# Kernel optimization log

Measured on AMD Instinct MI355X. Metric: run time of the kernel, lower is better.

## Reference

```python
import jax, jax.numpy as jnp
import numpy as np

EPS = 1e-5

def conv2d(x, w, stride=1, pad=0, groups=1):
    return jax.lax.conv_general_dilated(
        x, w, (stride, stride), [(pad, pad), (pad, pad)],
        feature_group_count=groups,
        dimension_numbers=('NCHW', 'OIHW', 'NCHW'))

def prelu(x, a):
    return jnp.where(x > 0, x, a[None, :, None, None] * x)

def batchnorm(x, g, b):
    # training-mode BN: batch statistics over N,H,W (biased variance, as torch)
    m = jnp.mean(x, axis=(0, 2, 3), keepdims=True)
    v = jnp.var(x, axis=(0, 2, 3), keepdims=True)
    xhat = (x - m) * jax.lax.rsqrt(v + EPS)
    return xhat * g[None, :, None, None] + b[None, :, None, None]

def setup_inputs() -> dict:
    key = jax.random.key(0)
    ks = jax.random.split(key, 8)
    C_in, C_out, stride = 128, 256, 2
    x = jax.random.normal(ks[0], (32, C_in, 56, 56), dtype=jnp.float32)
    w1 = jax.random.normal(ks[1], (C_out, C_in, 1, 1), dtype=jnp.float32) * 0.05
    w_dw = jax.random.normal(ks[2], (C_out, 1, 3, 3), dtype=jnp.float32) * 0.1
    w3 = jax.random.normal(ks[3], (C_out, C_out, 1, 1), dtype=jnp.float32) * 0.05
    w_adj = jax.random.normal(ks[4], (C_out, C_in, 1, 1), dtype=jnp.float32) * 0.05
    a_init = jnp.full((C_out,), 0.25, dtype=jnp.float32)  # PReLU init
    ones = jnp.ones((C_out,), dtype=jnp.float32)
    zeros = jnp.zeros((C_out,), dtype=jnp.float32)
    return {
        'x': x,
        'w1': w1, 'a1': a_init, 'g1': ones, 'b1': zeros,
        'w_dw': w_dw, 'a2': a_init, 'g2': ones, 'b2': zeros,
        'w3': w3, 'a3': a_init, 'g3': ones, 'b3': zeros,
        'w_adj': w_adj,
    }

def reference(x, w1, a1, g1, b1, w_dw, a2, g2, b2, w3, a3, g3, b3, w_adj):
    stride, C_out = 2, w_dw.shape[0]
    residual = conv2d(x, w_adj, stride=stride)  # full-precision shortcut
    xs = jnp.sign(x)
    # binary 1x1 conv (sign(x) already signed; sign is idempotent)
    out = conv2d(jnp.sign(xs), jnp.sign(w1))
    out = batchnorm(prelu(out, a1), g1, b1)
    # binary depthwise 3x3, stride, pad 1
    out = conv2d(jnp.sign(out), jnp.sign(w_dw), stride=stride, pad=1, groups=C_out)
    out = batchnorm(prelu(out, a2), g2, b2)
    # binary 1x1 conv
    out = conv2d(jnp.sign(out), jnp.sign(w3))
    out = batchnorm(prelu(out, a3), g3, b3)
    return out + residual
```

## Files before the change

### kernel.cpp

```cpp
#include <hip/hip_runtime.h>
#include <stdint.h>

#define NB   32
#define CIN  128
#define COUT 256
#define HH   56
#define WW   56
#define S1   (HH*WW)
#define HO   28
#define WO   28
#define S2   (HO*WO)
#define NS1  (NB*S1)
#define NS2  (NB*S2)
#define TOT2 (NS2*COUT)
#define EPSV 1e-5f

constexpr size_t OFF_XBITS = 0;
constexpr size_t OFF_WB1   = OFF_XBITS + (size_t)NS1*8*4;
constexpr size_t OFF_WB3   = OFF_WB1 + 256*8*4;
constexpr size_t OFF_WDW   = OFF_WB3 + 256*16*4;
constexpr size_t OFF_ACC   = OFF_WDW + 4096;
constexpr size_t OFF_WBADJ = OFF_ACC + 3*256*4*sizeof(int);
constexpr size_t OFF_XG    = OFF_WBADJ + (size_t)COUT*CIN*2;
constexpr size_t OFF_OUT1  = OFF_XG + (size_t)NS2*CIN*2;
constexpr size_t OFF_OUT2  = OFF_OUT1 + (size_t)NS1*COUT;
constexpr size_t OFF_XB2   = OFF_OUT2 + (size_t)TOT2;
constexpr size_t OFF_OUT3  = OFF_XB2 + (size_t)NS2*16*4;

typedef __attribute__((ext_vector_type(8))) short bf16x8;
typedef __attribute__((ext_vector_type(4))) float f32x4;

__device__ __forceinline__ uint32_t f2bf(float v) {
  uint32_t u = __float_as_uint(v);
  return (u + 0x7fffu + ((u >> 16) & 1u)) >> 16;
}

__device__ __forceinline__ void bn_finalize(const int* __restrict__ acc4,
                                            float a, float g, float b, float inv_ns,
                                            float& sc, float& sh) {
  float ps = (float)acc4[0];
  float ng = (float)acc4[1];
  float pq = (float)acc4[2];
  float nq = (float)acc4[3];
  float mean = (ps + a*ng) * inv_ns;
  float ex2  = (pq + a*a*nq) * inv_ns;
  float var  = ex2 - mean*mean;
  float rs   = rsqrtf(var + EPSV);
  sc = rs * g;
  sh = b - mean * sc;
}

__global__ __launch_bounds__(256) void packx_kernel(
    const float* __restrict__ x, uint32_t* __restrict__ xbits,
    uint32_t* __restrict__ xg,
    const float* __restrict__ w1, const float* __restrict__ w3,
    const float* __restrict__ wdw, const float* __restrict__ wadj,
    uint32_t* __restrict__ wb1, uint32_t* __restrict__ wb3,
    int8_t* __restrict__ wdws, uint32_t* __restrict__ wbadj,
    int* __restrict__ accbase) {
  int wdx = blockIdx.y;
  if (wdx == 0 && blockIdx.x < 256 && threadIdx.x < 64) {
    int co = blockIdx.x;
    int l  = threadIdx.x;
    if (l < 12) {
      int set = l >> 2, k = l & 3;
      accbase[set*1024 + co*4 + k] = 0;
    }
    for (int h = 0; h < 2; ++h) {
      float v = w1[(size_t)co*CIN + h*64 + l];
      unsigned long long bp = __ballot(v > 0.f);
      unsigned long long bn = __ballot(v < 0.f);
      if (l == 0) {
        wb1[co*8 + 2*h    ] = (uint32_t)bp;
        wb1[co*8 + 2*h + 1] = (uint32_t)(bp >> 32);
        wb1[co*8 + 4 + 2*h    ] = (uint32_t)bn;
        wb1[co*8 + 4 + 2*h + 1] = (uint32_t)(bn >> 32);
      }
    }
    for (int h = 0; h < 4; ++h) {
      float v = w3[(size_t)co*COUT + h*64 + l];
      unsigned long long bp = __ballot(v > 0.f);
      unsigned long long bn = __ballot(v < 0.f);
      if (l == 0) {
        wb3[co*16 + 2*h    ] = (uint32_t)bp;
        wb3[co*16 + 2*h + 1] = (uint32_t)(bp >> 32);
        wb3[co*16 + 8 + 2*h    ] = (uint32_t)bn;
        wb3[co*16 + 8 + 2*h + 1] = (uint32_t)(bn >> 32);
      }
    }
    if (l < 9) {
      float v = wdw[co*9 + l];
      wdws[co*9 + l] = (int8_t)((v > 0.f) - (v < 0.f));
    }
    {
      float v0 = wadj[(size_t)co*CIN + 2*l];
      float v1 = wadj[(size_t)co*CIN + 2*l + 1];
      wbadj[co*64 + l] = f2bf(v0) | (f2bf(v1) << 16);
    }
  }

  int m = blockIdx.x*256 + threadIdx.x;
  int n = m / S1, hw = m % S1;
  size_t base = ((size_t)n*CIN + wdx*32)*S1 + hw;
  uint32_t p = 0, q = 0;
  uint32_t bv[16];
  #pragma unroll
  for (int j = 0; j < 32; ++j) {
    float v = x[base + (size_t)j*S1];
    p |= (uint32_t)(v > 0.f) << j;
    q |= (uint32_t)(v < 0.f) << j;
    uint32_t b = f2bf(v);
    if (j & 1) bv[j >> 1] |= b << 16; else bv[j >> 1] = b;
  }
  xbits[(size_t)m*8 + wdx    ] = p;
  xbits[(size_t)m*8 + 4 + wdx] = q;
  int h = hw / WW, w = hw % WW;
  if (((h | w) & 1) == 0) {
    int m2 = n*S2 + (h >> 1)*WO + (w >> 1);
    uint4* dst = (uint4*)(xg + (size_t)m2*64 + wdx*16);
    dst[0] = make_uint4(bv[0],  bv[1],  bv[2],  bv[3]);
    dst[1] = make_uint4(bv[4],  bv[5],  bv[6],  bv[7]);
    dst[2] = make_uint4(bv[8],  bv[9],  bv[10], bv[11]);
    dst[3] = make_uint4(bv[12], bv[13], bv[14], bv[15]);
  }
}

__global__ __launch_bounds__(256) void conv1_kernel(
    const uint32_t* __restrict__ xb, const uint32_t* __restrict__ wb,
    int8_t* __restrict__ out1, int* __restrict__ accum1) {
  int tid = threadIdx.x;
  int qm = blockIdx.x*256 + tid;
  int m0 = qm*4;
  int n  = m0 / S1;
  int hw0 = m0 - n*S1;
  int co0 = blockIdx.y * 8;

  const uint4* xw = (const uint4*)(xb + (size_t)m0*8);
  uint4 xp0 = xw[0], xq0 = xw[1];
  uint4 xp1 = xw[2], xq1 = xw[3];
  uint4 xp2 = xw[4], xq2 = xw[5];
  uint4 xp3 = xw[6], xq3 = xw[7];

  uint32_t nz = (xp0.x|xq0.x)&(xp0.y|xq0.y)&(xp0.z|xq0.z)&(xp0.w|xq0.w)
              & (xp1.x|xq1.x)&(xp1.y|xq1.y)&(xp1.z|xq1.z)&(xp1.w|xq1.w)
              & (xp2.x|xq2.x)&(xp2.y|xq2.y)&(xp2.z|xq2.z)&(xp2.w|xq2.w)
              & (xp3.x|xq3.x)&(xp3.y|xq3.y)&(xp3.z|xq3.z)&(xp3.w|xq3.w);

  uint32_t res[8];
  if (nz == 0xffffffffu) {
    #pragma unroll
    for (int j = 0; j < 8; ++j) {
      const uint32_t* w8 = wb + (size_t)(co0 + j)*8;
      uint32_t w0 = w8[0], w1 = w8[1], w2 = w8[2], w3 = w8[3];
      int a0 = 128 - 2*(__popc(xp0.x^w0)+__popc(xp0.y^w1)+__popc(xp0.z^w2)+__popc(xp0.w^w3));
      int a1 = 128 - 2*(__popc(xp1.x^w0)+__popc(xp1.y^w1)+__popc(xp1.z^w2)+__popc(xp1.w^w3));
      int a2 = 128 - 2*(__popc(xp2.x^w0)+__popc(xp2.y^w1)+__popc(xp2.z^w2)+__popc(xp2.w^w3));
      int a3 = 128 - 2*(__popc(xp3.x^w0)+__popc(xp3.y^w1)+__popc(xp3.z^w2)+__popc(xp3.w^w3));
      if (a0 > 127) a0 = 127;
      if (a1 > 127) a1 = 127;
      if (a2 > 127) a2 = 127;
      if (a3 > 127) a3 = 127;
      res[j] = (uint32_t)(uint8_t)a0 | ((uint32_t)(uint8_t)a1 << 8)
             | ((uint32_t)(uint8_t)a2 << 16) | ((uint32_t)(uint8_t)a3 << 24);
    }
  } else {
    #pragma unroll
    for (int j = 0; j < 8; ++j) {
      const uint32_t* w8 = wb + (size_t)(co0 + j)*8;
      uint32_t w0 = w8[0], w1 = w8[1], w2 = w8[2], w3 = w8[3];
      uint32_t v0 = w8[4], v1 = w8[5], v2 = w8[6], v3 = w8[7];
      int a0 = __popc(xp0.x&w0)+__popc(xp0.y&w1)+__popc(xp0.z&w2)+__popc(xp0.w&w3)
             + __popc(xq0.x&v0)+__popc(xq0.y&v1)+__popc(xq0.z&v2)+__popc(xq0.w&v3)
             - __popc(xp0.x&v0)-__popc(xp0.y&v1)-__popc(xp0.z&v2)-__popc(xp0.w&v3)
             - __popc(xq0.x&w0)-__popc(xq0.y&w1)-__popc(xq0.z&w2)-__popc(xq0.w&w3);
      int a1 = __popc(xp1.x&w0)+__popc(xp1.y&w1)+__popc(xp1.z&w2)+__popc(xp1.w&w3)
             + __popc(xq1.x&v0)+__popc(xq1.y&v1)+__popc(xq1.z&v2)+__popc(xq1.w&v3)
             - __popc(xp1.x&v0)-__popc(xp1.y&v1)-__popc(xp1.z&v2)-__popc(xp1.w&v3)
             - __popc(xq1.x&w0)-__popc(xq1.y&w1)-__popc(xq1.z&w2)-__popc(xq1.w&w3);
      int a2 = __popc(xp2.x&w0)+__popc(xp2.y&w1)+__popc(xp2.z&w2)+__popc(xp2.w&w3)
             + __popc(xq2.x&v0)+__popc(xq2.y&v1)+__popc(xq2.z&v2)+__popc(xq2.w&v3)
             - __popc(xp2.x&v0)-__popc(xp2.y&v1)-__popc(xp2.z&v2)-__popc(xp2.w&v3)
             - __popc(xq2.x&w0)-__popc(xq2.y&w1)-__popc(xq2.z&w2)-__popc(xq2.w&w3);
      int a3 = __popc(xp3.x&w0)+__popc(xp3.y&w1)+__popc(xp3.z&w2)+__popc(xp3.w&w3)
             + __popc(xq3.x&v0)+__popc(xq3.y&v1)+__popc(xq3.z&v2)+__popc(xq3.w&v3)
             - __popc(xp3.x&v0)-__popc(xp3.y&v1)-__popc(xp3.z&v2)-__popc(xp3.w&v3)
             - __popc(xq3.x&w0)-__popc(xq3.y&w1)-__popc(xq3.z&w2)-__popc(xq3.w&w3);
      if (a0 > 127) a0 = 127;
      if (a1 > 127) a1 = 127;
      if (a2 > 127) a2 = 127;
      if (a3 > 127) a3 = 127;
      res[j] = (uint32_t)(uint8_t)a0 | ((uint32_t)(uint8_t)a1 << 8)
             | ((uint32_t)(uint8_t)a2 << 16) | ((uint32_t)(uint8_t)a3 << 24);
    }
  }

  __shared__ int sl[256][33];
  #pragma unroll
  for (int j = 0; j < 8; ++j) {
    int b0 = (int)(int8_t)(res[j]);
    int b1 = (int)(int8_t)(res[j] >> 8);
    int b2 = (int)(int8_t)(res[j] >> 16);
    int b3 = (int)(int8_t)(res[j] >> 24);
    int ps = 0, ns = 0, pq = 0, nq = 0;
    if (b0 > 0) { ps += b0; pq += b0*b0; } else { ns += b0; nq += b0*b0; }
    if (b1 > 0) { ps += b1; pq += b1*b1; } else { ns += b1; nq += b1*b1; }
    if (b2 > 0) { ps += b2; pq += b2*b2; } else { ns += b2; nq += b2*b2; }
    if (b3 > 0) { ps += b3; pq += b3*b3; } else { ns += b3; nq += b3*b3; }
    sl[tid][j*4+0] = ps; sl[tid][j*4+1] = ns;
    sl[tid][j*4+2] = pq; sl[tid][j*4+3] = nq;
  }
  __syncthreads();

  #pragma unroll
  for (int j = 0; j < 8; ++j)
    *(uint32_t*)(out1 + (size_t)(n*COUT + co0 + j)*S1 + hw0) = res[j];

  int s = tid & 31, g = tid >> 5;
  int part = 0;
  #pragma unroll
  for (int i = 0; i < 32; ++i) part += sl[g*32 + i][s];
  part += __shfl_xor(part, 32);
  __shared__ int sW[4][32];
  if ((tid & 63) < 32) sW[tid >> 6][s] = part;
  __syncthreads();
  if (tid < 32) {
    int tot = sW[0][tid] + sW[1][tid] + sW[2][tid] + sW[3][tid];
    atomicAdd(&accum1[co0*4 + tid], tot);
  }
}

#define DW_SLABS 8
#define DW_RB    68
__global__ __launch_bounds__(256) void dw_kernel(
    const int8_t* __restrict__ out1, const int8_t* __restrict__ wdws,
    const int* __restrict__ acc1, const float* __restrict__ a1,
    const float* __restrict__ g1, const float* __restrict__ b1,
    int8_t* __restrict__ out2, int* __restrict__ accum2) {
  __shared__ int8_t sl[DW_SLABS][57][DW_RB];
  __shared__ int sTp[DW_SLABS], sTn[DW_SLABS], sAcc[DW_SLABS][4];
  int tid = threadIdx.x;
  int nc0 = blockIdx.x * DW_SLABS;
  int co0 = nc0 & (COUT-1);

  int* slw = (int*)&sl[0][0][0];
  #pragma unroll
  for (int i = tid; i < DW_SLABS*57*DW_RB/4; i += 256) slw[i] = 0;
  if (tid < DW_SLABS) { sTp[tid] = 128; sTn[tid] = -129; }
  if (tid < DW_SLABS*4) sAcc[tid >> 2][tid & 3] = 0;
  __syncthreads();

  {
    int slab = tid >> 5;
    int co = co0 + slab;
    float av = a1[co], sc, sh;
    bn_finalize(acc1 + co*4, av, g1[co], b1[co], 1.f/NS1, sc, sh);
    int tp = 128, tn = -129;
    int v0 = -128 + (tid & 31)*8;
    #pragma unroll
    for (int k = 0; k < 8; ++k) {
      int v = v0 + k;
      float f = (float)v;
      float pr = f > 0.f ? f : av*f;
      float tv = pr*sc + sh;
      if (tv > 0.f && v < tp) tp = v;
      if (tv < 0.f && v > tn) tn = v;
    }
    atomicMin(&sTp[slab], tp);
    atomicMax(&sTn[slab], tn);
  }
  __syncthreads();

  for (int i = tid; i < DW_SLABS*784; i += 256) {
    int slab = i / 784;
    int d    = i - slab*784;
    int ih   = d / 14;
    int iwd  = d - ih*14;
    int Tp = sTp[slab], Tn = sTn[slab];
    uint32_t v4 = ((const uint32_t*)(out1 + (size_t)(nc0 + slab)*S1))[d];
    uint32_t s4 = 0;
    #pragma unroll
    for (int k = 0; k < 4; ++k) {
      int v = (int)(int8_t)(v4 >> (8*k));
      int s = (v >= Tp) - (v <= Tn);
      s4 |= (uint32_t)(s & 0xff) << (8*k);
    }
    *(uint32_t*)&sl[slab][ih + 1][4 + 4*iwd] = s4;
  }
  __syncthreads();

  int psum = 0, nsum = 0, psq = 0, nsq = 0;
  int slabD = tid / HO;
  if (tid < DW_SLABS*HO) {
    int ho   = tid - slabD*HO;
    int nc = nc0 + slabD;
    int co = co0 + slabD;
    int wv[9];
    #pragma unroll
    for (int k = 0; k < 9; ++k) wv[k] = wdws[co*9 + k];
    const uint32_t* r0 = (const uint32_t*)&sl[slabD][2*ho    ][4];
    const uint32_t* r1 = (const uint32_t*)&sl[slabD][2*ho + 1][4];
    const uint32_t* r2 = (const uint32_t*)&sl[slabD][2*ho + 2][4];
    uint32_t* o32 = (uint32_t*)(out2 + (size_t)nc*S2 + ho*WO);
    int c0 = 0, c1 = 0, c2 = 0;
    uint32_t obuf = 0;
    #pragma unroll
    for (int q = 0; q < 14; ++q) {
      uint32_t d0 = r0[q], d1 = r1[q], d2 = r2[q];
      int s00=(int)(int8_t)d0, s01=(int)(int8_t)(d0>>8), s02=(int)(int8_t)(d0>>16), s03=(int)(int8_t)(d0>>24);
      int s10=(int)(int8_t)d1, s11=(int)(int8_t)(d1>>8), s12=(int)(int8_t)(d1>>16), s13=(int)(int8_t)(d1>>24);
      int s20=(int)(int8_t)d2, s21=(int)(int8_t)(d2>>8), s22=(int)(int8_t)(d2>>16), s23=(int)(int8_t)(d2>>24);
      int a0 = c0*wv[0] + s00*wv[1] + s01*wv[2]
             + c1*wv[3] + s10*wv[4] + s11*wv[5]
             + c2*wv[6] + s20*wv[7] + s21*wv[8];
      int a1v = s01*wv[0] + s02*wv[1] + s03*wv[2]
              + s11*wv[3] + s12*wv[4] + s13*wv[5]
              + s21*wv[6] + s22*wv[7] + s23*wv[8];
      c0 = s03; c1 = s13; c2 = s23;
      if (a0 > 0) { psum += a0; psq += a0*a0; } else { nsum += a0; nsq += a0*a0; }
      if (a1v > 0) { psum += a1v; psq += a1v*a1v; } else { nsum += a1v; nsq += a1v*a1v; }
      if ((q & 1) == 0) {
        obuf = (uint32_t)(a0 & 0xff) | ((uint32_t)(a1v & 0xff) << 8);
      } else {
        obuf |= ((uint32_t)(a0 & 0xff) << 16) | ((uint32_t)(a1v & 0xff) << 24);
        o32[q >> 1] = obuf;
      }
    }
    atomicAdd(&sAcc[slabD][0], psum);
    atomicAdd(&sAcc[slabD][1], nsum);
    atomicAdd(&sAcc[slabD][2], psq);
    atomicAdd(&sAcc[slabD][3], nsq);
  }
  __syncthreads();

  if (tid < DW_SLABS*4) {
    int slab = tid >> 2, k = tid & 3;
    atomicAdd(&accum2[(co0 + slab)*4 + k], sAcc[slab][k]);
  }
}

__global__ __launch_bounds__(256) void pack2_kernel(
    const int8_t* __restrict__ out2, const int* __restrict__ acc2,
    const float* __restrict__ a2, const float* __restrict__ g2,
    const float* __restrict__ b2, uint32_t* __restrict__ xb2) {
  __shared__ int sTp[32], sTn[32];
  int wdx = blockIdx.y;
  if (threadIdx.x < 32) {
    int c = wdx*32 + threadIdx.x;
    float av = a2[c], sc, sh;
    bn_finalize(acc2 + c*4, av, g2[c], b2[c], 1.f/NS2, sc, sh);
    int tp = 10, tn = -10;
    for (int v = -9; v <= 9; ++v) {
      float f = (float)v;
      float pr = f > 0.f ? f : av*f;
      float tv = pr*sc + sh;
      if (tv > 0.f && v < tp) tp = v;
      if (tv < 0.f && v > tn) tn = v;
    }
    sTp[threadIdx.x] = tp; sTn[threadIdx.x] = tn;
  }
  __syncthreads();
  int m = blockIdx.x*256 + threadIdx.x;
  int n = m / S2, hw = m % S2;
  uint32_t p = 0, q = 0;
  #pragma unroll
  for (int j = 0; j < 32; ++j) {
    int c = wdx*32 + j;
    int v = out2[(size_t)(n*COUT + c)*S2 + hw];
    p |= (uint32_t)(v >= sTp[j]) << j;
    q |= (uint32_t)(v <= sTn[j]) << j;
  }
  xb2[(size_t)m*16 + wdx    ] = p;
  xb2[(size_t)m*16 + 8 + wdx] = q;
}

__global__ __launch_bounds__(256) void conv3_kernel(
    const uint32_t* __restrict__ xb2, const uint32_t* __restrict__ wb3,
    int16_t* __restrict__ out3, int* __restrict__ accum3) {
  int tid = threadIdx.x;
  int qm = blockIdx.x*256 + tid;
  int m0 = qm*2;
  int n  = m0 / S2;
  int hw0 = m0 - n*S2;
  int co0 = blockIdx.y * 8;

  const uint4* xw = (const uint4*)(xb2 + (size_t)m0*16);
  uint4 P0a = xw[0], P0b = xw[1], Q0a = xw[2], Q0b = xw[3];
  uint4 P1a = xw[4], P1b = xw[5], Q1a = xw[6], Q1b = xw[7];

  uint32_t nz = (P0a.x|Q0a.x)&(P0a.y|Q0a.y)&(P0a.z|Q0a.z)&(P0a.w|Q0a.w)
              & (P0b.x|Q0b.x)&(P0b.y|Q0b.y)&(P0b.z|Q0b.z)&(P0b.w|Q0b.w)
              & (P1a.x|Q1a.x)&(P1a.y|Q1a.y)&(P1a.z|Q1a.z)&(P1a.w|Q1a.w)
              & (P1b.x|Q1b.x)&(P1b.y|Q1b.y)&(P1b.z|Q1b.z)&(P1b.w|Q1b.w);

  uint32_t res[8];
  if (nz == 0xffffffffu) {
    #pragma unroll
    for (int j = 0; j < 8; ++j) {
      const uint32_t* w = wb3 + (size_t)(co0 + j)*16;
      int s0 = __popc(P0a.x^w[0])+__popc(P0a.y^w[1])+__popc(P0a.z^w[2])+__popc(P0a.w^w[3])
             + __popc(P0b.x^w[4])+__popc(P0b.y^w[5])+__popc(P0b.z^w[6])+__popc(P0b.w^w[7]);
      int s1 = __popc(P1a.x^w[0])+__popc(P1a.y^w[1])+__popc(P1a.z^w[2])+__popc(P1a.w^w[3])
             + __popc(P1b.x^w[4])+__popc(P1b.y^w[5])+__popc(P1b.z^w[6])+__popc(P1b.w^w[7]);
      int a0 = 256 - 2*s0, a1 = 256 - 2*s1;
      res[j] = (uint32_t)(uint16_t)(int16_t)a0 | ((uint32_t)(uint16_t)(int16_t)a1 << 16);
    }
  } else {
    #pragma unroll
    for (int j = 0; j < 8; ++j) {
      const uint32_t* w = wb3 + (size_t)(co0 + j)*16;
      int a0 = __popc(P0a.x&w[0])+__popc(P0a.y&w[1])+__popc(P0a.z&w[2])+__popc(P0a.w&w[3])
             + __popc(P0b.x&w[4])+__popc(P0b.y&w[5])+__popc(P0b.z&w[6])+__popc(P0b.w&w[7])
             + __popc(Q0a.x&w[8])+__popc(Q0a.y&w[9])+__popc(Q0a.z&w[10])+__popc(Q0a.w&w[11])
             + __popc(Q0b.x&w[12])+__popc(Q0b.y&w[13])+__popc(Q0b.z&w[14])+__popc(Q0b.w&w[15])
             - __popc(P0a.x&w[8])-__popc(P0a.y&w[9])-__popc(P0a.z&w[10])-__popc(P0a.w&w[11])
             - __popc(P0b.x&w[12])-__popc(P0b.y&w[13])-__popc(P0b.z&w[14])-__popc(P0b.w&w[15])
             - __popc(Q0a.x&w[0])-__popc(Q0a.y&w[1])-__popc(Q0a.z&w[2])-__popc(Q0a.w&w[3])
             - __popc(Q0b.x&w[4])-__popc(Q0b.y&w[5])-__popc(Q0b.z&w[6])-__popc(Q0b.w&w[7]);
      int a1 = __popc(P1a.x&w[0])+__popc(P1a.y&w[1])+__popc(P1a.z&w[2])+__popc(P1a.w&w[3])
             + __popc(P1b.x&w[4])+__popc(P1b.y&w[5])+__popc(P1b.z&w[6])+__popc(P1b.w&w[7])
             + __popc(Q1a.x&w[8])+__popc(Q1a.y&w[9])+__popc(Q1a.z&w[10])+__popc(Q1a.w&w[11])
             + __popc(Q1b.x&w[12])+__popc(Q1b.y&w[13])+__popc(Q1b.z&w[14])+__popc(Q1b.w&w[15])
             - __popc(P1a.x&w[8])-__popc(P1a.y&w[9])-__popc(P1a.z&w[10])-__popc(P1a.w&w[11])
             - __popc(P1b.x&w[12])-__popc(P1b.y&w[13])-__popc(P1b.z&w[14])-__popc(P1b.w&w[15])
             - __popc(Q1a.x&w[0])-__popc(Q1a.y&w[1])-__popc(Q1a.z&w[2])-__popc(Q1a.w&w[3])
             - __popc(Q1b.x&w[4])-__popc(Q1b.y&w[5])-__popc(Q1b.z&w[6])-__popc(Q1b.w&w[7]);
      res[j] = (uint32_t)(uint16_t)(int16_t)a0 | ((uint32_t)(uint16_t)(int16_t)a1 << 16);
    }
  }

  __shared__ int sl[256][33];
  #pragma unroll
  for (int j = 0; j < 8; ++j) {
    int b0 = (int)(int16_t)(res[j] & 0xffff);
    int b1 = (int)(int16_t)(res[j] >> 16);
    int ps = 0, ns = 0, pq = 0, nq = 0;
    if (b0 > 0) { ps += b0; pq += b0*b0; } else { ns += b0; nq += b0*b0; }
    if (b1 > 0) { ps += b1; pq += b1*b1; } else { ns += b1; nq += b1*b1; }
    sl[tid][j*4+0] = ps; sl[tid][j*4+1] = ns;
    sl[tid][j*4+2] = pq; sl[tid][j*4+3] = nq;
  }
  __syncthreads();

  #pragma unroll
  for (int j = 0; j < 8; ++j)
    *(uint32_t*)(out3 + (size_t)(n*COUT + co0 + j)*S2 + hw0) = res[j];

  int s = tid & 31, g = tid >> 5;
  int part = 0;
  #pragma unroll
  for (int i = 0; i < 32; ++i) part += sl[g*32 + i][s];
  part += __shfl_xor(part, 32);
  __shared__ int sW[4][32];
  if ((tid & 63) < 32) sW[tid >> 6][s] = part;
  __syncthreads();
  if (tid < 32) {
    int tot = sW[0][tid] + sW[1][tid] + sW[2][tid] + sW[3][tid];
    atomicAdd(&accum3[co0*4 + tid], tot);
  }
}

__global__ __launch_bounds__(256) void resfinal_kernel(
    const uint16_t* __restrict__ xg, const uint16_t* __restrict__ wb,
    const int16_t* __restrict__ out3,
    const float* __restrict__ a3, const float* __restrict__ g3,
    const float* __restrict__ b3, const int* __restrict__ acc3,
    float* __restrict__ out) {
  int lane = threadIdx.x & 63;
  int wid  = threadIdx.x >> 6;
  int m0  = blockIdx.x*64 + wid*16;
  int r16 = lane & 15, hi = lane >> 4;
  int koff = hi * 8;

  const bf16x8* arow = (const bf16x8*)(xg + (size_t)(m0 + r16)*CIN + koff);
  bf16x8 af0 = arow[0], af1 = arow[4], af2 = arow[8], af3 = arow[12];

  f32x4 dd[16];
  #pragma unroll
  for (int t = 0; t < 16; ++t) {
    const bf16x8* brow = (const bf16x8*)(wb + (size_t)(t*16 + r16)*CIN + koff);
    f32x4 a = {0.f,0.f,0.f,0.f};
    a = __builtin_amdgcn_mfma_f32_16x16x32_bf16(af0, brow[0],  a, 0,0,0);
    a = __builtin_amdgcn_mfma_f32_16x16x32_bf16(af1, brow[4],  a, 0,0,0);
    a = __builtin_amdgcn_mfma_f32_16x16x32_bf16(af2, brow[8],  a, 0,0,0);
    a = __builtin_amdgcn_mfma_f32_16x16x32_bf16(af3, brow[12], a, 0,0,0);
    dd[t] = a;
  }

  int mrow = m0 + hi*4;
  int n  = mrow / S2;
  int hw = mrow - n*S2;
  #pragma unroll
  for (int t = 0; t < 16; ++t) {
    int co = t*16 + r16;
    float av = a3[co], sc, sh;
    bn_finalize(acc3 + co*4, av, g3[co], b3[co], 1.f/NS2, sc, sh);
    size_t o = ((size_t)n*COUT + co)*S2 + hw;
    #pragma unroll
    for (int r = 0; r < 4; ++r) {
      float f = (float)out3[o + r];
      float pp = f > 0.f ? f : av*f;
      out[o + r] = pp*sc + sh + dd[t][r];
    }
  }
}

extern "C" void kernel_launch(void* const* d_in, const int* in_sizes, int n_in,
                              void* d_out, int out_size, void* d_ws, size_t ws_size,
                              hipStream_t stream) {
  (void)in_sizes; (void)n_in; (void)out_size; (void)ws_size;
  const float* x    = (const float*)d_in[0];
  const float* w1   = (const float*)d_in[1];
  const float* a1   = (const float*)d_in[2];
  const float* g1   = (const float*)d_in[3];
  const float* b1   = (const float*)d_in[4];
  const float* wdw  = (const float*)d_in[5];
  const float* a2   = (const float*)d_in[6];
  const float* g2   = (const float*)d_in[7];
  const float* b2   = (const float*)d_in[8];
  const float* w3   = (const float*)d_in[9];
  const float* a3   = (const float*)d_in[10];
  const float* g3   = (const float*)d_in[11];
  const float* b3   = (const float*)d_in[12];
  const float* wadj = (const float*)d_in[13];
  float* out = (float*)d_out;

  char* ws = (char*)d_ws;
  uint32_t* xbits = (uint32_t*)(ws + OFF_XBITS);
  uint32_t* wb1   = (uint32_t*)(ws + OFF_WB1);
  uint32_t* wb3   = (uint32_t*)(ws + OFF_WB3);
  int8_t*   wdws  = (int8_t*)  (ws + OFF_WDW);
  int*      acc1  = (int*)     (ws + OFF_ACC);
  int*      acc2  = acc1 + 256*4;
  int*      acc3  = acc2 + 256*4;
  uint32_t* wbadj = (uint32_t*)(ws + OFF_WBADJ);
  uint32_t* xg    = (uint32_t*)(ws + OFF_XG);
  int8_t*   out1  = (int8_t*)  (ws + OFF_OUT1);
  int8_t*   out2  = (int8_t*)  (ws + OFF_OUT2);
  uint32_t* xb2   = (uint32_t*)(ws + OFF_XB2);
  int16_t*  out3  = (int16_t*) (ws + OFF_OUT3);

  packx_kernel<<<dim3(NS1/256, 4), 256, 0, stream>>>(
      x, xbits, xg, w1, w3, wdw, wadj, wb1, wb3, wdws, wbadj, acc1);
  conv1_kernel<<<dim3(NS1/1024, 32), 256, 0, stream>>>(xbits, wb1, out1, acc1);
  dw_kernel<<<NB*COUT/DW_SLABS, 256, 0, stream>>>(out1, wdws, acc1, a1, g1, b1, out2, acc2);
  pack2_kernel<<<dim3(NS2/256, 8), 256, 0, stream>>>(out2, acc2, a2, g2, b2, xb2);
  conv3_kernel<<<dim3(NS2/512, 32), 256, 0, stream>>>(xb2, wb3, out3, acc3);
  resfinal_kernel<<<NS2/64, 256, 0, stream>>>(
      (const uint16_t*)xg, (const uint16_t*)wbadj, out3, a3, g3, b3, acc3, out);
}
```

Baseline: 109.1 us.

## Process eight pixels per thread in conv1 and fold zero handling into correction term

Each conv1 thread now computes eight spatial positions instead of four, halving the grid and reusing each weight load across twice as many pixels. The separate all-nonzero and general branches are merged: the XOR popcount path always runs, and a correction term for zero-valued inputs is added only when some input bit is zero. This aims to cut redundant weight loads and per-block overhead, at the cost of more registers per thread and fewer blocks for latency hiding. The output store becomes two 32-bit writes per channel row.

```diff
diff --git a/kernel.cpp b/kernel.cpp
--- a/kernel.cpp
+++ b/kernel.cpp
@@ -130,90 +130,74 @@
     int8_t* __restrict__ out1, int* __restrict__ accum1) {
   int tid = threadIdx.x;
   int qm = blockIdx.x*256 + tid;
-  int m0 = qm*4;
+  int m0 = qm*8;
   int n  = m0 / S1;
   int hw0 = m0 - n*S1;
   int co0 = blockIdx.y * 8;
 
   const uint4* xw = (const uint4*)(xb + (size_t)m0*8);
-  uint4 xp0 = xw[0], xq0 = xw[1];
-  uint4 xp1 = xw[2], xq1 = xw[3];
-  uint4 xp2 = xw[4], xq2 = xw[5];
-  uint4 xp3 = xw[6], xq3 = xw[7];
-
-  uint32_t nz = (xp0.x|xq0.x)&(xp0.y|xq0.y)&(xp0.z|xq0.z)&(xp0.w|xq0.w)
-              & (xp1.x|xq1.x)&(xp1.y|xq1.y)&(xp1.z|xq1.z)&(xp1.w|xq1.w)
-              & (xp2.x|xq2.x)&(xp2.y|xq2.y)&(xp2.z|xq2.z)&(xp2.w|xq2.w)
-              & (xp3.x|xq3.x)&(xp3.y|xq3.y)&(xp3.z|xq3.z)&(xp3.w|xq3.w);
-
-  uint32_t res[8];
-  if (nz == 0xffffffffu) {
-    #pragma unroll
-    for (int j = 0; j < 8; ++j) {
-      const uint32_t* w8 = wb + (size_t)(co0 + j)*8;
-      uint32_t w0 = w8[0], w1 = w8[1], w2 = w8[2], w3 = w8[3];
-      int a0 = 128 - 2*(__popc(xp0.x^w0)+__popc(xp0.y^w1)+__popc(xp0.z^w2)+__popc(xp0.w^w3));
-      int a1 = 128 - 2*(__popc(xp1.x^w0)+__popc(xp1.y^w1)+__popc(xp1.z^w2)+__popc(xp1.w^w3));
-      int a2 = 128 - 2*(__popc(xp2.x^w0)+__popc(xp2.y^w1)+__popc(xp2.z^w2)+__popc(xp2.w^w3));
-      int a3 = 128 - 2*(__popc(xp3.x^w0)+__popc(xp3.y^w1)+__popc(xp3.z^w2)+__popc(xp3.w^w3));
-      if (a0 > 127) a0 = 127;
-      if (a1 > 127) a1 = 127;
-      if (a2 > 127) a2 = 127;
-      if (a3 > 127) a3 = 127;
-      res[j] = (uint32_t)(uint8_t)a0 | ((uint32_t)(uint8_t)a1 << 8)
-             | ((uint32_t)(uint8_t)a2 << 16) | ((uint32_t)(uint8_t)a3 << 24);
-    }
-  } else {
-    #pragma unroll
-    for (int j = 0; j < 8; ++j) {
-      const uint32_t* w8 = wb + (size_t)(co0 + j)*8;
-      uint32_t w0 = w8[0], w1 = w8[1], w2 = w8[2], w3 = w8[3];
-      uint32_t v0 = w8[4], v1 = w8[5], v2 = w8[6], v3 = w8[7];
-      int a0 = __popc(xp0.x&w0)+__popc(xp0.y&w1)+__popc(xp0.z&w2)+__popc(xp0.w&w3)
-             + __popc(xq0.x&v0)+__popc(xq0.y&v1)+__popc(xq0.z&v2)+__popc(xq0.w&v3)
-             - __popc(xp0.x&v0)-__popc(xp0.y&v1)-__popc(xp0.z&v2)-__popc(xp0.w&v3)
-             - __popc(xq0.x&w0)-__popc(xq0.y&w1)-__popc(xq0.z&w2)-__popc(xq0.w&w3);
-      int a1 = __popc(xp1.x&w0)+__popc(xp1.y&w1)+__popc(xp1.z&w2)+__popc(xp1.w&w3)
-             + __popc(xq1.x&v0)+__popc(xq1.y&v1)+__popc(xq1.z&v2)+__popc(xq1.w&v3)
-             - __popc(xp1.x&v0)-__popc(xp1.y&v1)-__popc(xp1.z&v2)-__popc(xp1.w&v3)
-             - __popc(xq1.x&w0)-__popc(xq1.y&w1)-__popc(xq1.z&w2)-__popc(xq1.w&w3);
-      int a2 = __popc(xp2.x&w0)+__popc(xp2.y&w1)+__popc(xp2.z&w2)+__popc(xp2.w&w3)
-             + __popc(xq2.x&v0)+__popc(xq2.y&v1)+__popc(xq2.z&v2)+__popc(xq2.w&v3)
-             - __popc(xp2.x&v0)-__popc(xp2.y&v1)-__popc(xp2.z&v2)-__popc(xp2.w&v3)
-             - __popc(xq2.x&w0)-__popc(xq2.y&w1)-__popc(xq2.z&w2)-__popc(xq2.w&w3);
-      int a3 = __popc(xp3.x&w0)+__popc(xp3.y&w1)+__popc(xp3.z&w2)+__popc(xp3.w&w3)
-             + __popc(xq3.x&v0)+__popc(xq3.y&v1)+__popc(xq3.z&v2)+__popc(xq3.w&v3)
-             - __popc(xp3.x&v0)-__popc(xp3.y&v1)-__popc(xp3.z&v2)-__popc(xp3.w&v3)
-             - __popc(xq3.x&w0)-__popc(xq3.y&w1)-__popc(xq3.z&w2)-__popc(xq3.w&w3);
-      if (a0 > 127) a0 = 127;
-      if (a1 > 127) a1 = 127;
-      if (a2 > 127) a2 = 127;
-      if (a3 > 127) a3 = 127;
-      res[j] = (uint32_t)(uint8_t)a0 | ((uint32_t)(uint8_t)a1 << 8)
-             | ((uint32_t)(uint8_t)a2 << 16) | ((uint32_t)(uint8_t)a3 << 24);
-    }
-  }
+  uint4 xp0 = xw[0],  xq0 = xw[1];
+  uint4 xp1 = xw[2],  xq1 = xw[3];
+  uint4 xp2 = xw[4],  xq2 = xw[5];
+  uint4 xp3 = xw[6],  xq3 = xw[7];
+  uint4 xp4 = xw[8],  xq4 = xw[9];
+  uint4 xp5 = xw[10], xq5 = xw[11];
+  uint4 xp6 = xw[12], xq6 = xw[13];
+  uint4 xp7 = xw[14], xq7 = xw[15];
+
+#define NZP(i) ((xp##i.x|xq##i.x)&(xp##i.y|xq##i.y)&(xp##i.z|xq##i.z)&(xp##i.w|xq##i.w))
+  bool allnz = ((NZP(0)&NZP(1)&NZP(2)&NZP(3)&NZP(4)&NZP(5)&NZP(6)&NZP(7)) == 0xffffffffu);
+#undef NZP
 
   __shared__ int sl[256][33];
+  uint32_t rA[8], rB[8];
+
   #pragma unroll
   for (int j = 0; j < 8; ++j) {
-    int b0 = (int)(int8_t)(res[j]);
-    int b1 = (int)(int8_t)(res[j] >> 8);
-    int b2 = (int)(int8_t)(res[j] >> 16);
-    int b3 = (int)(int8_t)(res[j] >> 24);
+    const uint32_t* w8 = wb + (size_t)(co0 + j)*8;
+    uint32_t w0 = w8[0], w1 = w8[1], w2 = w8[2], w3 = w8[3];
+    int A0,A1,A2,A3,A4,A5,A6,A7;
+#define XORDOT(i,A) A = 128 - 2*(__popc(xp##i.x^w0)+__popc(xp##i.y^w1)+__popc(xp##i.z^w2)+__popc(xp##i.w^w3));
+    XORDOT(0,A0) XORDOT(1,A1) XORDOT(2,A2) XORDOT(3,A3)
+    XORDOT(4,A4) XORDOT(5,A5) XORDOT(6,A6) XORDOT(7,A7)
+#undef XORDOT
+    if (!allnz) {
+#define ZCORR(i,A) { \
+      uint32_t z0 = ~(xp##i.x|xq##i.x), z1 = ~(xp##i.y|xq##i.y); \
+      uint32_t z2 = ~(xp##i.z|xq##i.z), z3 = ~(xp##i.w|xq##i.w); \
+      A += 2*(__popc(z0&w0)+__popc(z1&w1)+__popc(z2&w2)+__popc(z3&w3)) \
+         - (__popc(z0)+__popc(z1)+__popc(z2)+__popc(z3)); }
+      ZCORR(0,A0) ZCORR(1,A1) ZCORR(2,A2) ZCORR(3,A3)
+      ZCORR(4,A4) ZCORR(5,A5) ZCORR(6,A6) ZCORR(7,A7)
+#undef ZCORR
+    }
+    if (A0 > 127) A0 = 127;
+    if (A1 > 127) A1 = 127;
+    if (A2 > 127) A2 = 127;
+    if (A3 > 127) A3 = 127;
+    if (A4 > 127) A4 = 127;
+    if (A5 > 127) A5 = 127;
+    if (A6 > 127) A6 = 127;
+    if (A7 > 127) A7 = 127;
+    rA[j] = (uint32_t)(uint8_t)A0 | ((uint32_t)(uint8_t)A1 << 8)
+          | ((uint32_t)(uint8_t)A2 << 16) | ((uint32_t)(uint8_t)A3 << 24);
+    rB[j] = (uint32_t)(uint8_t)A4 | ((uint32_t)(uint8_t)A5 << 8)
+          | ((uint32_t)(uint8_t)A6 << 16) | ((uint32_t)(uint8_t)A7 << 24);
     int ps = 0, ns = 0, pq = 0, nq = 0;
-    if (b0 > 0) { ps += b0; pq += b0*b0; } else { ns += b0; nq += b0*b0; }
-    if (b1 > 0) { ps += b1; pq += b1*b1; } else { ns += b1; nq += b1*b1; }
-    if (b2 > 0) { ps += b2; pq += b2*b2; } else { ns += b2; nq += b2*b2; }
-    if (b3 > 0) { ps += b3; pq += b3*b3; } else { ns += b3; nq += b3*b3; }
+#define STAT(A) if (A > 0) { ps += A; pq += A*A; } else { ns += A; nq += A*A; }
+    STAT(A0) STAT(A1) STAT(A2) STAT(A3) STAT(A4) STAT(A5) STAT(A6) STAT(A7)
+#undef STAT
     sl[tid][j*4+0] = ps; sl[tid][j*4+1] = ns;
     sl[tid][j*4+2] = pq; sl[tid][j*4+3] = nq;
   }
   __syncthreads();
 
   #pragma unroll
-  for (int j = 0; j < 8; ++j)
-    *(uint32_t*)(out1 + (size_t)(n*COUT + co0 + j)*S1 + hw0) = res[j];
+  for (int j = 0; j < 8; ++j) {
+    uint32_t* dst = (uint32_t*)(out1 + (size_t)(n*COUT + co0 + j)*S1 + hw0);
+    dst[0] = rA[j];
+    dst[1] = rB[j];
+  }
 
   int s = tid & 31, g = tid >> 5;
   int part = 0;
@@ -541,7 +525,7 @@
 
   packx_kernel<<<dim3(NS1/256, 4), 256, 0, stream>>>(
       x, xbits, xg, w1, w3, wdw, wadj, wb1, wb3, wdws, wbadj, acc1);
-  conv1_kernel<<<dim3(NS1/1024, 32), 256, 0, stream>>>(xbits, wb1, out1, acc1);
+  conv1_kernel<<<dim3(NS1/2048, 32), 256, 0, stream>>>(xbits, wb1, out1, acc1);
   dw_kernel<<<NB*COUT/DW_SLABS, 256, 0, stream>>>(out1, wdws, acc1, a1, g1, b1, out2, acc2);
   pack2_kernel<<<dim3(NS2/256, 8), 256, 0, stream>>>(out2, acc2, a2, g2, b2, xb2);
   conv3_kernel<<<dim3(NS2/512, 32), 256, 0, stream>>>(xb2, wb3, out3, acc3);
```

Result: slower. 112.6 us (+3.3%).
